# Kernel tuning notes

Hardware: AMD Instinct MI355X
Metric: run time of the kernel (lower is better)

The kernel has to match this reference:

```python
import jax, jax.numpy as jnp
import numpy as np

N, E, C, H, T, R = 32768, 262144, 128, 8, 8, 8
DK = C // H


def _typed_linear(feat, W, b, tid):
    # per-type linear: rows with tid==t get feat @ W[t] + b[t]; others untouched base 0
    out = jnp.zeros((feat.shape[0], W.shape[-1]), feat.dtype)
    for t in range(W.shape[0]):
        m = (tid == t)[:, None]
        out = jnp.where(m, feat @ W[t] + b[t], out)
    return out


def _forward(x, type_id, edge_index, edge_attr, Wk, bk, Wq, bq, Wv, bv, Wa, ba,
             relation_pri, relation_att, relation_msg, skip, gamma, beta):
    n, c = x.shape
    r, h, dk, _ = relation_att.shape
    src, dst = edge_index[0], edge_index[1]
    fs, fd = x[src], x[dst]                      # [E, C] gathers
    # per-edge-type k/q/v projections (source masks by edge_attr)
    k = _typed_linear(fs, Wk, bk, edge_attr).reshape(-1, h, dk)
    q = _typed_linear(fd, Wq, bq, edge_attr).reshape(-1, h, dk)
    v = _typed_linear(fs, Wv, bv, edge_attr).reshape(-1, h, dk)
    # relation transforms without materializing [E,h,dk,dk] gathers
    kt = jnp.zeros_like(k)
    vt = jnp.zeros_like(v)
    for ri in range(r):
        m = (edge_attr == ri)[:, None, None]
        kt = jnp.where(m, jnp.einsum('ehd,hdk->ehk', k, relation_att[ri]), kt)
        vt = jnp.where(m, jnp.einsum('ehd,hdk->ehk', v, relation_msg[ri]), vt)
    pri = relation_pri[edge_attr]                # [E, H]
    att = (q * kt).sum(-1) * pri / jnp.sqrt(jnp.asarray(dk, x.dtype))  # [E, H]
    # scatter softmax over destination-node groups
    mx = jax.ops.segment_max(att, dst, num_segments=n)
    ex = jnp.exp(att - mx[dst])
    den = jax.ops.segment_sum(ex, dst, num_segments=n)
    a = ex / den[dst]                            # [E, H]
    w = (a[..., None] * vt).reshape(-1, h * dk)  # [E, C]
    # scatter mean into node slots (zeros for isolated nodes)
    s = jax.ops.segment_sum(w, dst, num_segments=n)
    cnt = jax.ops.segment_sum(jnp.ones((w.shape[0], 1), x.dtype), dst, num_segments=n)
    x0 = jnp.where(cnt > 0, s / jnp.maximum(cnt, 1.0), 0.0)
    # per-node-type output projection + gated residual
    x0 = _typed_linear(x0, Wa, ba, type_id)
    alpha = jax.nn.sigmoid(skip)[type_id][:, None]
    out = x0 * alpha + x * (1.0 - alpha)
    # type-indexed LayerNorm (eps = 1e-5), dropout is identity in eval
    mu = out.mean(-1, keepdims=True)
    var = ((out - mu) ** 2).mean(-1, keepdims=True)
    xn = (out - mu) / jnp.sqrt(var + 1e-5)
    return xn * gamma[type_id] + beta[type_id]


def setup_inputs() -> dict:
    key = jax.random.key(0)
    ks = jax.random.split(key, 16)
    w = 1.0 / np.sqrt(C)
    wr = 1.0 / np.sqrt(DK)
    return {
        'x': jax.random.normal(ks[0], (N, C), jnp.float32),
        'type_id': jax.random.randint(ks[1], (N,), 0, T),
        'edge_index': jax.random.randint(ks[2], (2, E), 0, N),
        'edge_attr': jax.random.randint(ks[3], (E,), 0, R),
        'Wk': jax.random.normal(ks[4], (T, C, C), jnp.float32) * w,
        'bk': jax.random.normal(ks[5], (T, C), jnp.float32) * 0.02,
        'Wq': jax.random.normal(ks[6], (T, C, C), jnp.float32) * w,
        'bq': jax.random.normal(ks[7], (T, C), jnp.float32) * 0.02,
        'Wv': jax.random.normal(ks[8], (T, C, C), jnp.float32) * w,
        'bv': jax.random.normal(ks[9], (T, C), jnp.float32) * 0.02,
        'Wa': jax.random.normal(ks[10], (T, C, C), jnp.float32) * w,
        'ba': jax.random.normal(ks[11], (T, C), jnp.float32) * 0.02,
        'relation_pri': jnp.ones((R, H), jnp.float32),
        'relation_att': jax.random.normal(ks[12], (R, H, DK, DK), jnp.float32) * wr,
        'relation_msg': jax.random.normal(ks[13], (R, H, DK, DK), jnp.float32) * wr,
        'skip': jnp.ones((T,), jnp.float32),
        'gamma': jnp.ones((T, C), jnp.float32),
        'beta': jnp.zeros((T, C), jnp.float32),
    }


def reference(x, type_id, edge_index, edge_attr, Wk, bk, Wq, bq, Wv, bv, Wa, ba,
              relation_pri, relation_att, relation_msg, skip, gamma, beta):
    return _forward(x, type_id, edge_index, edge_attr, Wk, bk, Wq, bq, Wv, bv, Wa, ba,
                    relation_pri, relation_att, relation_msg, skip, gamma, beta)
```

## Files before the change

kernel.cpp:

```cpp
#include <hip/hip_runtime.h>
#include <math.h>

#define NN 32768
#define NE 262144
#define CD 128
#define NH 8
#define NT 8
#define NR 8

typedef unsigned short u16;
typedef unsigned long long ull;
typedef __attribute__((ext_vector_type(8))) short bhalf8;
typedef __attribute__((ext_vector_type(4))) short short4v;
typedef __attribute__((ext_vector_type(4))) float f32x4;


__device__ __forceinline__ u16 f2b(float f) {
    union { float f; unsigned u; } v; v.f = f;
    unsigned r = v.u + 0x7FFF + ((v.u >> 16) & 1);
    return (u16)(r >> 16);
}
__device__ __forceinline__ float b2f(unsigned h) {
    union { unsigned u; float f; } v; v.u = h << 16;
    return v.f;
}

#define PREP_BLOCKS 2057

__global__ void prep_zero(const float* __restrict__ Wk, const float* __restrict__ bk,
                          const float* __restrict__ Wq,
                          const float* __restrict__ Wv, const float* __restrict__ bv,
                          const float* __restrict__ Wa,
                          const float* __restrict__ Aatt, const float* __restrict__ Amsg,
                          u16* __restrict__ WqT, u16* __restrict__ WkT,
                          u16* __restrict__ WvT, u16* __restrict__ WaT,
                          float* __restrict__ bkf, float* __restrict__ bvf,
                          int* __restrict__ degd) {
    if (blockIdx.x >= PREP_BLOCKS) {
        int zi = (blockIdx.x - PREP_BLOCKS) * 256 + threadIdx.x;
        if (zi < 2 * NN) degd[zi] = 0;
        return;
    }
    const int WCNT = NT * CD * CD;
    int idx = blockIdx.x * 256 + threadIdx.x;
    if (idx < 4 * WCNT) {
        int mat = idx >> 17;
        int o = idx & (WCNT - 1);
        int t = o >> 14;
        int n = (o >> 7) & 127;
        int k = o & 127;
        int ct = n >> 4, lx2 = n & 15, kk = k >> 5, qd = (k >> 3) & 3, dd = k & 7;
        int oo = t * 16384 + (((ct * 4 + kk) * 4 + qd) * 16 + lx2) * 8 + dd;
        if (mat == 0) {
            WqT[oo] = f2b(Wq[(t * CD + k) * CD + n]);
        } else if (mat == 3) {
            WaT[oo] = f2b(Wa[(t * CD + k) * CD + n]);
        } else {
            int h = n >> 4, j = n & 15;
            const float* W = (mat == 1) ? Wk : Wv;
            const float* A = (mat == 1) ? Aatt : Amsg;
            const float* wrow = W + (t * CD + k) * CD + h * 16;
            const float* acol = A + ((t * NH + h) * 16) * 16 + j;
            float s = 0.f;
#pragma unroll
            for (int d = 0; d < 16; ++d) s += wrow[d] * acol[d * 16];
            ((mat == 1) ? WkT : WvT)[oo] = f2b(s);
        }
    } else {
        int o2 = idx - 4 * WCNT;
        if (o2 < 2 * NT * CD) {
            int which = (o2 >= NT * CD) ? 1 : 0;
            int o = o2 - which * NT * CD;
            const float* B = which ? bv : bk;
            const float* A = which ? Amsg : Aatt;
            int t = o >> 7; int c = o & 127; int h = c >> 4; int j = c & 15;
            const float* brow = B + t * CD + h * 16;
            const float* acol = A + ((t * NH + h) * 16) * 16 + j;
            float s = 0.f;
#pragma unroll
            for (int d = 0; d < 16; ++d) s += brow[d] * acol[d * 16];
            (which ? bvf : bkf)[o] = s;
        }
    }
}

__global__ void hists(const int* __restrict__ ea, const int* __restrict__ tidv,
                      const int* __restrict__ dstv,
                      int* __restrict__ epart, int* __restrict__ npart,
                      int* __restrict__ deg) {
    __shared__ int wc[4][8];
    const int b = blockIdx.x;
    const int tid = threadIdx.x;
    const int lane = tid & 63, w = tid >> 6;
    int i = b * 256 + tid;
    int t = ea[i];
    atomicAdd(&deg[dstv[i]], 1);
#pragma unroll
    for (int u = 0; u < 8; ++u) {
        ull m = __ballot(t == u);
        if (lane == 0) wc[w][u] = __popcll(m);
    }
    __syncthreads();
    if (tid < 8) epart[b * 8 + tid] = wc[0][tid] + wc[1][tid] + wc[2][tid] + wc[3][tid];
    if (b < NN / 256) {
        int tn = tidv[i];
        __syncthreads();
#pragma unroll
        for (int u = 0; u < 8; ++u) {
            ull m = __ballot(tn == u);
            if (lane == 0) wc[w][u] = __popcll(m);
        }
        __syncthreads();
        if (tid < 8) npart[b * 8 + tid] = wc[0][tid] + wc[1][tid] + wc[2][tid] + wc[3][tid];
    }
}

__launch_bounds__(1024)
__global__ void scan_all(const int* __restrict__ deg, int* __restrict__ dbase,
                         int* __restrict__ epart, int* __restrict__ npart,
                         int* __restrict__ ectr, int* __restrict__ nctr) {
    const int t = threadIdx.x;
    if (blockIdx.x == 0) {
        __shared__ int part[1024];
        int local[32];
        int s = 0;
#pragma unroll
        for (int i = 0; i < 32; ++i) { local[i] = s; s += deg[t * 32 + i]; }
        part[t] = s;
        __syncthreads();
        for (int off = 1; off < 1024; off <<= 1) {
            int v = (t >= off) ? part[t - off] : 0;
            __syncthreads();
            part[t] += v;
            __syncthreads();
        }
        int base = (t == 0) ? 0 : part[t - 1];
#pragma unroll
        for (int i = 0; i < 32; ++i) dbase[t * 32 + i] = base + local[i];
        return;
    }
    __shared__ int sc[1024 * 8];
    int v[8], orig[8];
#pragma unroll
    for (int u = 0; u < 8; ++u) { orig[u] = v[u] = epart[t * 8 + u]; sc[t * 8 + u] = v[u]; }
    for (int off = 1; off < 1024; off <<= 1) {
        __syncthreads();
        int wv[8];
        bool p = (t >= off);
        if (p) {
#pragma unroll
            for (int u = 0; u < 8; ++u) wv[u] = sc[(t - off) * 8 + u];
        }
        __syncthreads();
        if (p) {
#pragma unroll
            for (int u = 0; u < 8; ++u) { v[u] += wv[u]; sc[t * 8 + u] = v[u]; }
        }
    }
    __syncthreads();
    int tot[8], base[8];
    {
        int acc = 0;
#pragma unroll
        for (int u = 0; u < 8; ++u) { tot[u] = sc[1023 * 8 + u]; base[u] = acc; acc += tot[u]; }
    }
#pragma unroll
    for (int u = 0; u < 8; ++u) epart[t * 8 + u] = base[u] + v[u] - orig[u];
    if (t == 0) {
        ectr[8] = 0; ectr[17] = 0;
        int acc = 0, ptb = 0;
        for (int u = 0; u < 8; ++u) {
            acc += tot[u]; ectr[9 + u] = acc;
            ptb += (tot[u] + 63) >> 6; ectr[18 + u] = ptb;
        }
    }
    __syncthreads();
    int nv[8], nor[8];
#pragma unroll
    for (int u = 0; u < 8; ++u) {
        nor[u] = nv[u] = (t < 128) ? npart[t * 8 + u] : 0;
        sc[t * 8 + u] = nv[u];
    }
    for (int off = 1; off < 128; off <<= 1) {
        __syncthreads();
        int wv[8];
        bool p = (t >= off && t < 128);
        if (p) {
#pragma unroll
            for (int u = 0; u < 8; ++u) wv[u] = sc[(t - off) * 8 + u];
        }
        __syncthreads();
        if (p) {
#pragma unroll
            for (int u = 0; u < 8; ++u) { nv[u] += wv[u]; sc[t * 8 + u] = nv[u]; }
        }
    }
    __syncthreads();
    int ntot[8], nbase[8];
    {
        int acc = 0;
#pragma unroll
        for (int u = 0; u < 8; ++u) { ntot[u] = sc[127 * 8 + u]; nbase[u] = acc; acc += ntot[u]; }
    }
    if (t < 128) {
#pragma unroll
        for (int u = 0; u < 8; ++u) npart[t * 8 + u] = nbase[u] + nv[u] - nor[u];
    }
    if (t == 0) {
        nctr[8] = 0; nctr[17] = 0;
        int acc = 0, ptb = 0;
        for (int u = 0; u < 8; ++u) {
            acc += ntot[u]; nctr[9 + u] = acc;
            ptb += (ntot[u] + 63) >> 6; nctr[18 + u] = ptb;
        }
    }
}

__global__ void scatter2(const int* __restrict__ ea, const int* __restrict__ tidv,
                         const int* __restrict__ epart, const int* __restrict__ npart,
                         int* __restrict__ eperm, int* __restrict__ nperm) {
    __shared__ int wc[4][8];
    __shared__ int wo[4][8];
    const int b = blockIdx.x;
    const int tid = threadIdx.x;
    const int lane = tid & 63, w = tid >> 6;
    const int* lab; const int* off; int* perm; int i;
    if (b < NE / 256) { lab = ea; off = epart + b * 8; perm = eperm; i = b * 256 + tid; }
    else { lab = tidv; off = npart + (b - NE / 256) * 8; perm = nperm; i = (b - NE / 256) * 256 + tid; }
    int t = lab[i];
    const ull below = (1ull << lane) - 1;
    int myrank = 0;
#pragma unroll
    for (int u = 0; u < 8; ++u) {
        ull m = __ballot(t == u);
        if (lane == 0) wc[w][u] = __popcll(m);
        if (t == u) myrank = __popcll(m & below);
    }
    __syncthreads();
    if (tid < 32) {
        int u = tid & 7, w2 = tid >> 3;
        int s = 0;
        for (int w3 = 0; w3 < w2; ++w3) s += wc[w3][u];
        wo[w2][u] = s;
    }
    __syncthreads();
    perm[off[t] + wo[w][t] + myrank] = i;
}

__device__ __forceinline__ void gemm64g(const u16* __restrict__ sA,
                                        const u16* __restrict__ gW,
                                        int rh, int ch, int lx, int quad, int lane,
                                        const float* __restrict__ biasRow,
                                        f32x4 acc[2][4]) {
#pragma unroll
    for (int nt = 0; nt < 4; ++nt) {
        float bv = biasRow[ch * 64 + nt * 16 + lx];
        acc[0][nt] = f32x4{bv, bv, bv, bv};
        acc[1][nt] = f32x4{bv, bv, bv, bv};
    }
    const int m0 = rh * 32 + lx;
    const u16* wbase = gW + (ch * 4) * 2048 + lane * 8;
    bhalf8 bb[2][4];
#pragma unroll
    for (int nt = 0; nt < 4; ++nt)
        bb[0][nt] = *(const bhalf8*)(wbase + nt * 2048);
#pragma unroll
    for (int kk = 0; kk < 4; ++kk) {
        if (kk < 3) {
#pragma unroll
            for (int nt = 0; nt < 4; ++nt)
                bb[(kk + 1) & 1][nt] = *(const bhalf8*)(wbase + nt * 2048 + (kk + 1) * 512);
        }
        const int ko = kk * 32 + quad * 8;
        bhalf8 a0 = *(const bhalf8*)&sA[m0 * 136 + ko];
        bhalf8 a1 = *(const bhalf8*)&sA[(m0 + 16) * 136 + ko];
#pragma unroll
        for (int nt = 0; nt < 4; ++nt) {
            acc[0][nt] = __builtin_amdgcn_mfma_f32_16x16x32_bf16(a0, bb[kk & 1][nt], acc[0][nt], 0, 0, 0);
            acc[1][nt] = __builtin_amdgcn_mfma_f32_16x16x32_bf16(a1, bb[kk & 1][nt], acc[1][nt], 0, 0, 0);
        }
    }
}

__launch_bounds__(256, 4)
__global__ void edge_kernel(const float* __restrict__ x,
                            const int* __restrict__ src, const int* __restrict__ dst,
                            const u16* __restrict__ WqT, const float* __restrict__ bq,
                            const u16* __restrict__ WkT, const float* __restrict__ bkf,
                            const u16* __restrict__ WvT, const float* __restrict__ bvf,
                            const float* __restrict__ pri,
                            const int* __restrict__ ectr, const int* __restrict__ eperm,
                            const int* __restrict__ dbase, int* __restrict__ dcur,
                            float* __restrict__ exs, u16* __restrict__ vts) {
    __shared__ u16 sFS[64 * 136];
    __shared__ u16 sFD[64 * 136];
    __shared__ int sSrc[64], sDst[64], sPos[64];

    const int tid = threadIdx.x;
    const int lane = tid & 63;
    const int w = tid >> 6;
    const int lx = lane & 15;
    const int quad = lane >> 4;
    const int ch = w & 1;
    const int rh = w >> 1;
    const int b = blockIdx.x;

    int t = -1, lt = 0;
#pragma unroll
    for (int u = 0; u < NR; ++u) {
        int p0 = ectr[17 + u], p1 = ectr[18 + u];
        if (b >= p0 && b < p1) { t = u; lt = b - p0; }
    }
    if (t < 0) return;
    const int base = ectr[8 + t];
    const int sz = ectr[9 + t] - base;
    const int start = lt * 64;

    if (tid < 64) {
        int idx = start + tid;
        int e = (idx < sz) ? eperm[base + idx] : -1;
        int valid = (e >= 0) ? 1 : 0;
        int d = valid ? dst[e] : 0;
        sSrc[tid] = valid ? src[e] : 0;
        sDst[tid] = d;
        sPos[tid] = valid ? (dbase[d] + atomicAdd(&dcur[d], 1)) : NE;
    }
    __syncthreads();

#pragma unroll
    for (int it = 0; it < 8; ++it) {
        int c = tid + it * 256;
        int row = c >> 5, c4 = c & 31;
        float4 v = *((const float4*)(x + (long)sSrc[row] * CD) + c4);
        short4v pk; pk.x = (short)f2b(v.x); pk.y = (short)f2b(v.y);
        pk.z = (short)f2b(v.z); pk.w = (short)f2b(v.w);
        *(short4v*)&sFS[row * 136 + c4 * 4] = pk;
        float4 u2 = *((const float4*)(x + (long)sDst[row] * CD) + c4);
        short4v pk2; pk2.x = (short)f2b(u2.x); pk2.y = (short)f2b(u2.y);
        pk2.z = (short)f2b(u2.z); pk2.w = (short)f2b(u2.w);
        *(short4v*)&sFD[row * 136 + c4 * 4] = pk2;
    }
    __syncthreads();

    f32x4 qa[2][4], ka[2][4];
    gemm64g(sFD, WqT + t * 16384, rh, ch, lx, quad, lane, bq + t * CD, qa);
    gemm64g(sFS, WkT + t * 16384, rh, ch, lx, quad, lane, bkf + t * CD, ka);

    float ex[2][4][4];
#pragma unroll
    for (int nt = 0; nt < 4; ++nt) {
        const float ph = pri[t * NH + ch * 4 + nt] * 0.25f;
#pragma unroll
        for (int mt = 0; mt < 2; ++mt) {
#pragma unroll
            for (int reg = 0; reg < 4; ++reg) {
                float p = qa[mt][nt][reg] * ka[mt][nt][reg];
                p += __shfl_xor(p, 1);
                p += __shfl_xor(p, 2);
                p += __shfl_xor(p, 4);
                p += __shfl_xor(p, 8);
                ex[mt][nt][reg] = __expf(p * ph);
            }
        }
    }
    if (lx == 0) {
#pragma unroll
        for (int mt = 0; mt < 2; ++mt)
#pragma unroll
            for (int reg = 0; reg < 4; ++reg) {
                int erow = rh * 32 + mt * 16 + quad * 4 + reg;
                float4 e4 = {ex[mt][0][reg], ex[mt][1][reg], ex[mt][2][reg], ex[mt][3][reg]};
                *(float4*)(exs + (long)sPos[erow] * 8 + ch * 4) = e4;
            }
    }

    f32x4 va[2][4];
    gemm64g(sFS, WvT + t * 16384, rh, ch, lx, quad, lane, bvf + t * CD, va);
    __syncthreads();
#pragma unroll
    for (int mt = 0; mt < 2; ++mt)
#pragma unroll
        for (int reg = 0; reg < 4; ++reg) {
            int erow = rh * 32 + mt * 16 + quad * 4 + reg;
#pragma unroll
            for (int nt = 0; nt < 4; ++nt)
                sFD[erow * 136 + ch * 64 + nt * 16 + lx] = f2b(va[mt][nt][reg]);
        }
    __syncthreads();
#pragma unroll
    for (int it = 0; it < 4; ++it) {
        int c = tid + it * 256;
        int row = c >> 4, off = (c & 15) * 8;
        *(bhalf8*)&vts[(long)sPos[row] * 128 + off] = *(const bhalf8*)&sFD[row * 136 + off];
    }
}

__launch_bounds__(256, 4)
__global__ void node_kernel(const float* __restrict__ x,
                            const u16* __restrict__ WaT, const float* __restrict__ ba,
                            const float* __restrict__ skip, const float* __restrict__ gamma,
                            const float* __restrict__ beta,
                            const int* __restrict__ nctr, const int* __restrict__ nperm,
                            const int* __restrict__ dbase, const int* __restrict__ deg,
                            const float* __restrict__ exs, const u16* __restrict__ vts,
                            float* __restrict__ out) {
    __shared__ u16 sX0[64 * 136];
    __shared__ int sNode[64], sVal[64];

    const int tid = threadIdx.x;
    const int lane = tid & 63;
    const int w = tid >> 6;
    const int lx = lane & 15;
    const int quad = lane >> 4;
    const int b = blockIdx.x;

    int t = -1, lt = 0;
#pragma unroll
    for (int u = 0; u < NT; ++u) {
        int p0 = nctr[17 + u], p1 = nctr[18 + u];
        if (b >= p0 && b < p1) { t = u; lt = b - p0; }
    }
    if (t < 0) return;
    const int base = nctr[8 + t];
    const int sz = nctr[9 + t] - base;
    const int start = lt * 64;

    if (tid < 64) {
        int idx = start + tid;
        int n = (idx < sz) ? nperm[base + idx] : -1;
        sVal[tid] = (n >= 0) ? 1 : 0;
        sNode[tid] = (n >= 0) ? n : 0;
    }
    __syncthreads();

    for (int r4 = 0; r4 < 4; ++r4) {
        int row = w * 16 + r4 * 4 + quad;
        int n = sNode[row];
        int s = dbase[n], d = deg[n];
        const u16* vp = vts + (long)s * 128 + lx * 8;
        const float* ep = exs + (long)s * 8 + (lx >> 1);
        float a[8] = {0.f, 0.f, 0.f, 0.f, 0.f, 0.f, 0.f, 0.f};
        float sden = 0.f;
        int j = 0;
        for (; j + 2 <= d; j += 2) {
            bhalf8 v0 = *(const bhalf8*)(vp + (long)j * 128);
            bhalf8 v1 = *(const bhalf8*)(vp + (long)(j + 1) * 128);
            float e0 = ep[(long)j * 8];
            float e1 = ep[(long)(j + 1) * 8];
#pragma unroll
            for (int c = 0; c < 8; ++c)
                a[c] += e0 * b2f((u16)v0[c]) + e1 * b2f((u16)v1[c]);
            sden += e0 + e1;
        }
        if (j < d) {
            bhalf8 v0 = *(const bhalf8*)(vp + (long)j * 128);
            float e0 = ep[(long)j * 8];
#pragma unroll
            for (int c = 0; c < 8; ++c) a[c] += e0 * b2f((u16)v0[c]);
            sden += e0;
        }
        float inv = (d > 0) ? 1.f / (sden * (float)d) : 0.f;
        bhalf8 pk;
#pragma unroll
        for (int c = 0; c < 8; ++c) pk[c] = (short)f2b(a[c] * inv);
        *(bhalf8*)&sX0[row * 136 + lx * 8] = pk;
    }
    __syncthreads();

    f32x4 acc[8];
#pragma unroll
    for (int nt = 0; nt < 8; ++nt) {
        float bv = ba[t * CD + nt * 16 + lx];
        acc[nt] = f32x4{bv, bv, bv, bv};
    }
    const int m0 = w * 16 + lx;
    const u16* wbase = WaT + t * 16384 + lane * 8;
#pragma unroll
    for (int kk = 0; kk < 4; ++kk) {
        bhalf8 nb[8];
#pragma unroll
        for (int ct = 0; ct < 8; ++ct)
            nb[ct] = *(const bhalf8*)(wbase + ct * 2048 + kk * 512);
        bhalf8 a = *(const bhalf8*)&sX0[m0 * 136 + kk * 32 + quad * 8];
#pragma unroll
        for (int ct = 0; ct < 8; ++ct)
            acc[ct] = __builtin_amdgcn_mfma_f32_16x16x32_bf16(a, nb[ct], acc[ct], 0, 0, 0);
    }

    const float alpha = 1.f / (1.f + __expf(-skip[t]));
    const float oma = 1.f - alpha;
    float g[8], be[8];
#pragma unroll
    for (int nt = 0; nt < 8; ++nt) {
        g[nt] = gamma[t * CD + nt * 16 + lx];
        be[nt] = beta[t * CD + nt * 16 + lx];
    }
#pragma unroll
    for (int reg = 0; reg < 4; ++reg) {
        int erow = w * 16 + quad * 4 + reg;
        int n = sNode[erow];
        const float* xr = x + (long)n * CD;
        float o[8];
        float s1 = 0.f, s2 = 0.f;
#pragma unroll
        for (int nt = 0; nt < 8; ++nt) {
            float xv = xr[nt * 16 + lx];
            float ov = acc[nt][reg] * alpha + xv * oma;
            o[nt] = ov;
            s1 += ov;
            s2 += ov * ov;
        }
#pragma unroll
        for (int m = 1; m < 16; m <<= 1) {
            s1 += __shfl_xor(s1, m);
            s2 += __shfl_xor(s2, m);
        }
        float mu = s1 * (1.f / 128.f);
        float var = s2 * (1.f / 128.f) - mu * mu;
        float rs = rsqrtf(var + 1e-5f);
        if (sVal[erow]) {
            float* op = out + (long)n * CD;
#pragma unroll
            for (int nt = 0; nt < 8; ++nt)
                __builtin_nontemporal_store((o[nt] - mu) * rs * g[nt] + be[nt],
                                            &op[nt * 16 + lx]);
        }
    }
}

extern "C" void kernel_launch(void* const* d_in, const int* in_sizes, int n_in,
                              void* d_out, int out_size, void* d_ws, size_t ws_size,
                              hipStream_t stream) {
    const float* x        = (const float*)d_in[0];
    const int*   type_id  = (const int*)d_in[1];
    const int*   edge_idx = (const int*)d_in[2];
    const int*   edge_attr= (const int*)d_in[3];
    const float* Wk   = (const float*)d_in[4];
    const float* bk   = (const float*)d_in[5];
    const float* Wq   = (const float*)d_in[6];
    const float* bq   = (const float*)d_in[7];
    const float* Wv   = (const float*)d_in[8];
    const float* bv   = (const float*)d_in[9];
    const float* Wa   = (const float*)d_in[10];
    const float* ba   = (const float*)d_in[11];
    const float* pri  = (const float*)d_in[12];
    const float* Aatt = (const float*)d_in[13];
    const float* Amsg = (const float*)d_in[14];
    const float* skip = (const float*)d_in[15];
    const float* gam  = (const float*)d_in[16];
    const float* bet  = (const float*)d_in[17];

    char* ws = (char*)d_ws;
    u16*   WqT  = (u16*)(ws + 0);
    u16*   WkT  = (u16*)(ws + 262144);
    u16*   WvT  = (u16*)(ws + 524288);
    u16*   WaT  = (u16*)(ws + 786432);
    float* bkf  = (float*)(ws + 1048576);
    float* bvf  = (float*)(ws + 1052672);
    float* exs  = (float*)(ws + 1056768);
    u16*   vts  = (u16*)(ws + 9447424);
    int*   deg  = (int*)  (ws + 76572672);
    int*   dcur = (int*)  (ws + 76703744);
    int*   dbase= (int*)  (ws + 76834816);
    int*   eperm= (int*)  (ws + 76965888);
    int*   nperm= (int*)  (ws + 78014464);
    int*   ectr = (int*)  (ws + 78145536);
    int*   nctr = (int*)  (ws + 78145792);
    int*   epart= (int*)  (ws + 78146048);
    int*   npart= (int*)  (ws + 78178816);

    const int* src = edge_idx;
    const int* dst = edge_idx + NE;

    prep_zero<<<PREP_BLOCKS + 256, 256, 0, stream>>>(
        Wk, bk, Wq, Wv, bv, Wa, Aatt, Amsg, WqT, WkT, WvT, WaT, bkf, bvf, deg);
    hists<<<NE / 256, 256, 0, stream>>>(edge_attr, type_id, dst, epart, npart, deg);
    scan_all<<<2, 1024, 0, stream>>>(deg, dbase, epart, npart, ectr, nctr);
    scatter2<<<NE / 256 + NN / 256, 256, 0, stream>>>(edge_attr, type_id, epart, npart,
                                                      eperm, nperm);
    edge_kernel<<<NE / 64 + NR, 256, 0, stream>>>(x, src, dst, WqT, bq, WkT, bkf, WvT, bvf,
                                                  pri, ectr, eperm, dbase, dcur, exs, vts);
    node_kernel<<<NN / 64 + NT, 256, 0, stream>>>(x, WaT, ba, skip, gam, bet, nctr, nperm,
                                                  dbase, deg, exs, vts, (float*)d_out);
}
```

Baseline: 248.7 us.

## Pre-convert x to bf16, pack edge metadata in scatter, widen node gather

Converts x to bf16 once in the prep kernel so the edge kernel gathers half the bytes per row and skips per-edge conversion. The scatter pass now writes a packed int4 (src, dst, slot position) per sorted edge and does the dcur atomic there, which removes the dependent eperm→src/dst→dbase load chain from the edge kernel. The node aggregation is remapped so 8 lanes cover a row with 16 channels each, handling 8 rows per wave-step instead of 4. The cost is an extra 8 MB bf16 copy of x, a 4 MB packed edge array, and more work in scatter2.

```diff
diff --git a/kernel.cpp b/kernel.cpp
--- a/kernel.cpp
+++ b/kernel.cpp
@@ -11,7 +11,6 @@
 typedef unsigned short u16;
 typedef unsigned long long ull;
 typedef __attribute__((ext_vector_type(8))) short bhalf8;
-typedef __attribute__((ext_vector_type(4))) short short4v;
 typedef __attribute__((ext_vector_type(4))) float f32x4;
 
 
@@ -26,16 +25,32 @@
 }
 
 #define PREP_BLOCKS 2057
+#define ZB_BLOCKS 256
+#define XB_BLOCKS 2048
 
 __global__ void prep_zero(const float* __restrict__ Wk, const float* __restrict__ bk,
                           const float* __restrict__ Wq,
                           const float* __restrict__ Wv, const float* __restrict__ bv,
                           const float* __restrict__ Wa,
                           const float* __restrict__ Aatt, const float* __restrict__ Amsg,
+                          const float* __restrict__ x,
                           u16* __restrict__ WqT, u16* __restrict__ WkT,
                           u16* __restrict__ WvT, u16* __restrict__ WaT,
                           float* __restrict__ bkf, float* __restrict__ bvf,
-                          int* __restrict__ degd) {
+                          int* __restrict__ degd, u16* __restrict__ xb) {
+    if (blockIdx.x >= PREP_BLOCKS + ZB_BLOCKS) {
+        int zi = (blockIdx.x - PREP_BLOCKS - ZB_BLOCKS) * 256 + threadIdx.x;
+        long basei = (long)zi * 8;
+        float4 v0 = *(const float4*)(x + basei);
+        float4 v1 = *(const float4*)(x + basei + 4);
+        bhalf8 pk;
+        pk[0] = (short)f2b(v0.x); pk[1] = (short)f2b(v0.y);
+        pk[2] = (short)f2b(v0.z); pk[3] = (short)f2b(v0.w);
+        pk[4] = (short)f2b(v1.x); pk[5] = (short)f2b(v1.y);
+        pk[6] = (short)f2b(v1.z); pk[7] = (short)f2b(v1.w);
+        *(bhalf8*)(xb + basei) = pk;
+        return;
+    }
     if (blockIdx.x >= PREP_BLOCKS) {
         int zi = (blockIdx.x - PREP_BLOCKS) * 256 + threadIdx.x;
         if (zi < 2 * NN) degd[zi] = 0;
@@ -217,16 +232,19 @@
 }
 
 __global__ void scatter2(const int* __restrict__ ea, const int* __restrict__ tidv,
+                         const int* __restrict__ srcv, const int* __restrict__ dstv,
                          const int* __restrict__ epart, const int* __restrict__ npart,
-                         int* __restrict__ eperm, int* __restrict__ nperm) {
+                         const int* __restrict__ dbase, int* __restrict__ dcur,
+                         int4* __restrict__ epack, int* __restrict__ nperm) {
     __shared__ int wc[4][8];
     __shared__ int wo[4][8];
     const int b = blockIdx.x;
     const int tid = threadIdx.x;
     const int lane = tid & 63, w = tid >> 6;
-    const int* lab; const int* off; int* perm; int i;
-    if (b < NE / 256) { lab = ea; off = epart + b * 8; perm = eperm; i = b * 256 + tid; }
-    else { lab = tidv; off = npart + (b - NE / 256) * 8; perm = nperm; i = (b - NE / 256) * 256 + tid; }
+    const bool is_e = (b < NE / 256);
+    const int* lab; const int* off; int i;
+    if (is_e) { lab = ea; off = epart + b * 8; i = b * 256 + tid; }
+    else { lab = tidv; off = npart + (b - NE / 256) * 8; i = (b - NE / 256) * 256 + tid; }
     int t = lab[i];
     const ull below = (1ull << lane) - 1;
     int myrank = 0;
@@ -244,7 +262,14 @@
         wo[w2][u] = s;
     }
     __syncthreads();
-    perm[off[t] + wo[w][t] + myrank] = i;
+    int slot = off[t] + wo[w][t] + myrank;
+    if (is_e) {
+        int s = srcv[i], d = dstv[i];
+        int pos = dbase[d] + atomicAdd(&dcur[d], 1);
+        epack[slot] = int4{s, d, pos, 0};
+    } else {
+        nperm[slot] = i;
+    }
 }
 
 __device__ __forceinline__ void gemm64g(const u16* __restrict__ sA,
@@ -283,14 +308,12 @@
 }
 
 __launch_bounds__(256, 4)
-__global__ void edge_kernel(const float* __restrict__ x,
-                            const int* __restrict__ src, const int* __restrict__ dst,
+__global__ void edge_kernel(const u16* __restrict__ xb,
                             const u16* __restrict__ WqT, const float* __restrict__ bq,
                             const u16* __restrict__ WkT, const float* __restrict__ bkf,
                             const u16* __restrict__ WvT, const float* __restrict__ bvf,
                             const float* __restrict__ pri,
-                            const int* __restrict__ ectr, const int* __restrict__ eperm,
-                            const int* __restrict__ dbase, int* __restrict__ dcur,
+                            const int* __restrict__ ectr, const int4* __restrict__ epack,
                             float* __restrict__ exs, u16* __restrict__ vts) {
     __shared__ u16 sFS[64 * 136];
     __shared__ u16 sFD[64 * 136];
@@ -318,27 +341,19 @@
 
     if (tid < 64) {
         int idx = start + tid;
-        int e = (idx < sz) ? eperm[base + idx] : -1;
-        int valid = (e >= 0) ? 1 : 0;
-        int d = valid ? dst[e] : 0;
-        sSrc[tid] = valid ? src[e] : 0;
-        sDst[tid] = d;
-        sPos[tid] = valid ? (dbase[d] + atomicAdd(&dcur[d], 1)) : NE;
-    }
-    __syncthreads();
-
-#pragma unroll
-    for (int it = 0; it < 8; ++it) {
+        int4 pk = (idx < sz) ? epack[base + idx] : int4{0, 0, NE, 0};
+        sSrc[tid] = pk.x;
+        sDst[tid] = pk.y;
+        sPos[tid] = pk.z;
+    }
+    __syncthreads();
+
+#pragma unroll
+    for (int it = 0; it < 4; ++it) {
         int c = tid + it * 256;
-        int row = c >> 5, c4 = c & 31;
-        float4 v = *((const float4*)(x + (long)sSrc[row] * CD) + c4);
-        short4v pk; pk.x = (short)f2b(v.x); pk.y = (short)f2b(v.y);
-        pk.z = (short)f2b(v.z); pk.w = (short)f2b(v.w);
-        *(short4v*)&sFS[row * 136 + c4 * 4] = pk;
-        float4 u2 = *((const float4*)(x + (long)sDst[row] * CD) + c4);
-        short4v pk2; pk2.x = (short)f2b(u2.x); pk2.y = (short)f2b(u2.y);
-        pk2.z = (short)f2b(u2.z); pk2.w = (short)f2b(u2.w);
-        *(short4v*)&sFD[row * 136 + c4 * 4] = pk2;
+        int row = c >> 4, off = (c & 15) * 8;
+        *(bhalf8*)&sFS[row * 136 + off] = *(const bhalf8*)&xb[(long)sSrc[row] * CD + off];
+        *(bhalf8*)&sFD[row * 136 + off] = *(const bhalf8*)&xb[(long)sDst[row] * CD + off];
     }
     __syncthreads();
 
@@ -433,37 +448,55 @@
     }
     __syncthreads();
 
-    for (int r4 = 0; r4 < 4; ++r4) {
-        int row = w * 16 + r4 * 4 + quad;
-        int n = sNode[row];
-        int s = dbase[n], d = deg[n];
-        const u16* vp = vts + (long)s * 128 + lx * 8;
-        const float* ep = exs + (long)s * 8 + (lx >> 1);
-        float a[8] = {0.f, 0.f, 0.f, 0.f, 0.f, 0.f, 0.f, 0.f};
-        float sden = 0.f;
-        int j = 0;
-        for (; j + 2 <= d; j += 2) {
-            bhalf8 v0 = *(const bhalf8*)(vp + (long)j * 128);
-            bhalf8 v1 = *(const bhalf8*)(vp + (long)(j + 1) * 128);
-            float e0 = ep[(long)j * 8];
-            float e1 = ep[(long)(j + 1) * 8];
-#pragma unroll
-            for (int c = 0; c < 8; ++c)
-                a[c] += e0 * b2f((u16)v0[c]) + e1 * b2f((u16)v1[c]);
-            sden += e0 + e1;
-        }
-        if (j < d) {
-            bhalf8 v0 = *(const bhalf8*)(vp + (long)j * 128);
-            float e0 = ep[(long)j * 8];
-#pragma unroll
-            for (int c = 0; c < 8; ++c) a[c] += e0 * b2f((u16)v0[c]);
-            sden += e0;
-        }
-        float inv = (d > 0) ? 1.f / (sden * (float)d) : 0.f;
-        bhalf8 pk;
-#pragma unroll
-        for (int c = 0; c < 8; ++c) pk[c] = (short)f2b(a[c] * inv);
-        *(bhalf8*)&sX0[row * 136 + lx * 8] = pk;
+    {
+        const int sub = lane >> 3;
+        const int l8 = lane & 7;
+        for (int r2 = 0; r2 < 2; ++r2) {
+            int row = w * 16 + r2 * 8 + sub;
+            int n = sNode[row];
+            int s = dbase[n], d = deg[n];
+            const u16* vp = vts + (long)s * 128 + l8 * 16;
+            const float* ep = exs + (long)s * 8 + l8;
+            float a[16];
+#pragma unroll
+            for (int c = 0; c < 16; ++c) a[c] = 0.f;
+            float sden = 0.f;
+            int j = 0;
+            for (; j + 2 <= d; j += 2) {
+                bhalf8 v0a = *(const bhalf8*)(vp + (long)j * 128);
+                bhalf8 v0b = *(const bhalf8*)(vp + (long)j * 128 + 8);
+                bhalf8 v1a = *(const bhalf8*)(vp + (long)(j + 1) * 128);
+                bhalf8 v1b = *(const bhalf8*)(vp + (long)(j + 1) * 128 + 8);
+                float e0 = ep[(long)j * 8];
+                float e1 = ep[(long)(j + 1) * 8];
+#pragma unroll
+                for (int c = 0; c < 8; ++c) {
+                    a[c] += e0 * b2f((u16)v0a[c]) + e1 * b2f((u16)v1a[c]);
+                    a[8 + c] += e0 * b2f((u16)v0b[c]) + e1 * b2f((u16)v1b[c]);
+                }
+                sden += e0 + e1;
+            }
+            if (j < d) {
+                bhalf8 v0a = *(const bhalf8*)(vp + (long)j * 128);
+                bhalf8 v0b = *(const bhalf8*)(vp + (long)j * 128 + 8);
+                float e0 = ep[(long)j * 8];
+#pragma unroll
+                for (int c = 0; c < 8; ++c) {
+                    a[c] += e0 * b2f((u16)v0a[c]);
+                    a[8 + c] += e0 * b2f((u16)v0b[c]);
+                }
+                sden += e0;
+            }
+            float inv = (d > 0) ? 1.f / (sden * (float)d) : 0.f;
+            bhalf8 p0, p1;
+#pragma unroll
+            for (int c = 0; c < 8; ++c) {
+                p0[c] = (short)f2b(a[c] * inv);
+                p1[c] = (short)f2b(a[8 + c] * inv);
+            }
+            *(bhalf8*)&sX0[row * 136 + l8 * 16] = p0;
+            *(bhalf8*)&sX0[row * 136 + l8 * 16 + 8] = p1;
+        }
     }
     __syncthreads();
 
@@ -562,24 +595,26 @@
     int*   deg  = (int*)  (ws + 76572672);
     int*   dcur = (int*)  (ws + 76703744);
     int*   dbase= (int*)  (ws + 76834816);
-    int*   eperm= (int*)  (ws + 76965888);
     int*   nperm= (int*)  (ws + 78014464);
     int*   ectr = (int*)  (ws + 78145536);
     int*   nctr = (int*)  (ws + 78145792);
     int*   epart= (int*)  (ws + 78146048);
     int*   npart= (int*)  (ws + 78178816);
+    u16*   xb   = (u16*)  (ws + 78182912);
+    int4*  epack= (int4*) (ws + 86571520);
 
     const int* src = edge_idx;
     const int* dst = edge_idx + NE;
 
-    prep_zero<<<PREP_BLOCKS + 256, 256, 0, stream>>>(
-        Wk, bk, Wq, Wv, bv, Wa, Aatt, Amsg, WqT, WkT, WvT, WaT, bkf, bvf, deg);
+    prep_zero<<<PREP_BLOCKS + ZB_BLOCKS + XB_BLOCKS, 256, 0, stream>>>(
+        Wk, bk, Wq, Wv, bv, Wa, Aatt, Amsg, x, WqT, WkT, WvT, WaT, bkf, bvf, deg, xb);
     hists<<<NE / 256, 256, 0, stream>>>(edge_attr, type_id, dst, epart, npart, deg);
     scan_all<<<2, 1024, 0, stream>>>(deg, dbase, epart, npart, ectr, nctr);
-    scatter2<<<NE / 256 + NN / 256, 256, 0, stream>>>(edge_attr, type_id, epart, npart,
-                                                      eperm, nperm);
-    edge_kernel<<<NE / 64 + NR, 256, 0, stream>>>(x, src, dst, WqT, bq, WkT, bkf, WvT, bvf,
-                                                  pri, ectr, eperm, dbase, dcur, exs, vts);
+    scatter2<<<NE / 256 + NN / 256, 256, 0, stream>>>(edge_attr, type_id, src, dst,
+                                                      epart, npart, dbase, dcur,
+                                                      epack, nperm);
+    edge_kernel<<<NE / 64 + NR, 256, 0, stream>>>(xb, WqT, bq, WkT, bkf, WvT, bvf,
+                                                  pri, ectr, epack, exs, vts);
     node_kernel<<<NN / 64 + NT, 256, 0, stream>>>(x, WaT, ba, skip, gam, bet, nctr, nperm,
                                                   dbase, deg, exs, vts, (float*)d_out);
 }
```

Result: faster. 239.4 us (-3.7%).
